# Kernel optimization log

Measured on AMD Instinct MI355X. Metric: run time of the kernel, lower is better.

The kernel has to match this reference:

```python
import jax, jax.numpy as jnp
import numpy as np

EPS = 1e-5


def setup_inputs() -> dict:
    key = jax.random.key(0)
    ks = jax.random.split(key, 7)
    B, T, H = 4, 4096, 1024
    x = jax.random.normal(ks[0], (B, T, H), dtype=jnp.float32)
    gamma = jnp.ones((H,), dtype=jnp.float32)
    beta = jnp.zeros((H,), dtype=jnp.float32)
    s = 1.0 / np.sqrt(H)
    Wg = jax.random.uniform(ks[1], (H, H), minval=-s, maxval=s, dtype=jnp.float32)
    bg = jax.random.uniform(ks[2], (H,), minval=-s, maxval=s, dtype=jnp.float32)
    Wc = jax.random.uniform(ks[3], (H, H), minval=-s, maxval=s, dtype=jnp.float32)
    bc = jax.random.uniform(ks[4], (H,), minval=-s, maxval=s, dtype=jnp.float32)
    return {"x": x, "gamma": gamma, "beta": beta, "Wg": Wg, "bg": bg, "Wc": Wc, "bc": bc}


def reference(x, gamma, beta, Wg, bg, Wc, bc):
    # x: [B, T, H]
    mu = jnp.mean(x, axis=-1, keepdims=True)
    var = jnp.mean((x - mu) ** 2, axis=-1, keepdims=True)
    normed = (x - mu) * jax.lax.rsqrt(var + EPS) * gamma + beta
    z = jax.nn.sigmoid(jnp.einsum('bth,oh->bto', normed, Wg) + bg)  # gate
    c = jnp.einsum('bth,oh->bto', normed, Wc) + bc                  # candidate
    B, T, H = x.shape

    def step(h, zc):
        z_t, c_t = zc  # each [B, H]
        h = (1.0 - z_t) * h + z_t * c_t
        return h, h

    h0 = jnp.zeros((B, H), dtype=x.dtype)
    # scan over time: move T to leading axis
    _, hs = jax.lax.scan(step, h0, (jnp.swapaxes(z, 0, 1), jnp.swapaxes(c, 0, 1)))
    return jnp.swapaxes(hs, 0, 1) + x  # residual
```

## Files before the change

### kernel.cpp

```cpp
#include <hip/hip_runtime.h>
#include <stdint.h>


#define B_    4
#define T_    4096
#define H_    1024
#define BT_   (B_*T_)
#define EPSV  1e-5f
#define CHK   128
#define CL    (T_/CHK)

typedef float  f32x4  __attribute__((ext_vector_type(4)));
typedef __bf16 bf16x8 __attribute__((ext_vector_type(8)));
typedef unsigned short u16;

__device__ __forceinline__ u16 f2bf(float f) {
  uint32_t u = __builtin_bit_cast(uint32_t, f);
  u += 0x7fffu + ((u >> 16) & 1u);
  return (u16)(u >> 16);
}
__device__ __forceinline__ float bf2f(uint32_t u) {
  uint32_t v = (u & 0xffffu) << 16;
  return __builtin_bit_cast(float, v);
}
__device__ __forceinline__ void bf4(uint2 p, float* f) {
  f[0] = bf2f(p.x); f[1] = bf2f(p.x >> 16);
  f[2] = bf2f(p.y); f[3] = bf2f(p.y >> 16);
}

__global__ __launch_bounds__(256) void ln_kernel(
    const float* __restrict__ x, const float* __restrict__ gamma,
    const float* __restrict__ beta, u16* __restrict__ normed) {
  const int wid  = threadIdx.x >> 6, lane = threadIdx.x & 63;
  const int row  = blockIdx.x * 4 + wid;
  const float4* xr = reinterpret_cast<const float4*>(x + (size_t)row * H_);
  float4 v[4];
  float s = 0.0f, q = 0.0f;
  #pragma unroll
  for (int seg = 0; seg < 4; ++seg) {
    v[seg] = xr[seg * 64 + lane];
    s += v[seg].x + v[seg].y + v[seg].z + v[seg].w;
    q += v[seg].x*v[seg].x + v[seg].y*v[seg].y + v[seg].z*v[seg].z + v[seg].w*v[seg].w;
  }
  #pragma unroll
  for (int off = 1; off < 64; off <<= 1) {
    s += __shfl_xor(s, off);
    q += __shfl_xor(q, off);
  }
  const float mean = s * (1.0f / H_);
  const float var  = q * (1.0f / H_) - mean * mean;
  const float rstd = rsqrtf(var + EPSV);
  const float4* g4 = reinterpret_cast<const float4*>(gamma);
  const float4* b4 = reinterpret_cast<const float4*>(beta);
  uint2* o2 = reinterpret_cast<uint2*>(normed + (size_t)row * H_);
  #pragma unroll
  for (int seg = 0; seg < 4; ++seg) {
    const float4 g = g4[seg * 64 + lane];
    const float4 b = b4[seg * 64 + lane];
    uint2 o;
    o.x = (uint32_t)f2bf((v[seg].x - mean) * rstd * g.x + b.x)
        | ((uint32_t)f2bf((v[seg].y - mean) * rstd * g.y + b.y) << 16);
    o.y = (uint32_t)f2bf((v[seg].z - mean) * rstd * g.z + b.z)
        | ((uint32_t)f2bf((v[seg].w - mean) * rstd * g.w + b.w) << 16);
    o2[seg * 64 + lane] = o;
  }
}

__global__ __launch_bounds__(256) void pack_kernel(
    const float* __restrict__ Wg, const float* __restrict__ Wc,
    u16* __restrict__ wpack) {
  const int idx4 = (blockIdx.x * 256 + threadIdx.x) * 4;
  const int n = idx4 >> 10;
  const int k = idx4 & 1023;
  const float* src = (n < 1024) ? (Wg + (size_t)n * 1024 + k)
                                : (Wc + (size_t)(n - 1024) * 1024 + k);
  const float4 v = *reinterpret_cast<const float4*>(src);
  uint2 o;
  o.x = (uint32_t)f2bf(v.x) | ((uint32_t)f2bf(v.y) << 16);
  o.y = (uint32_t)f2bf(v.z) | ((uint32_t)f2bf(v.w) << 16);
  *reinterpret_cast<uint2*>(wpack + idx4) = o;
}

__global__ __launch_bounds__(256) void gemm_kernel(
    const u16* __restrict__ A, const u16* __restrict__ Bw,
    const float* __restrict__ bg, const float* __restrict__ bc,
    u16* __restrict__ zbuf, u16* __restrict__ cbuf) {
  __shared__ u16 As[2][128 * 32];
  __shared__ u16 Bs[2][128 * 32];
  const int bid = blockIdx.x;
  const int nb  = (bid & 7) * 256 + (bid >> 3);
  const int mt  = nb >> 4, nt = nb & 15;
  const int tid = threadIdx.x;
  const int wid = tid >> 6, lane = tid & 63;
  const int wr = wid >> 1, wcq = wid & 1;

  f32x4 acc[4][4] = {};

  const int c0 = tid, c1 = tid + 256;
  const u16* a0 = A  + (size_t)(mt * 128 + (c0 >> 2)) * 1024 + (c0 & 3) * 8;
  const u16* a1 = A  + (size_t)(mt * 128 + (c1 >> 2)) * 1024 + (c1 & 3) * 8;
  const u16* b0 = Bw + (size_t)(nt * 128 + (c0 >> 2)) * 1024 + (c0 & 3) * 8;
  const u16* b1 = Bw + (size_t)(nt * 128 + (c1 >> 2)) * 1024 + (c1 & 3) * 8;

  const int frow = lane & 15;
  const int kb   = (lane >> 4) * 8;

  auto stage = [&](int buf, int ks) {
    const int kk = ks * 32;
    __builtin_amdgcn_global_load_lds(
        (const __attribute__((address_space(1))) void*)(a0 + kk),
        (__attribute__((address_space(3))) void*)&As[buf][c0 * 8], 16, 0, 0);
    __builtin_amdgcn_global_load_lds(
        (const __attribute__((address_space(1))) void*)(a1 + kk),
        (__attribute__((address_space(3))) void*)&As[buf][c1 * 8], 16, 0, 0);
    __builtin_amdgcn_global_load_lds(
        (const __attribute__((address_space(1))) void*)(b0 + kk),
        (__attribute__((address_space(3))) void*)&Bs[buf][c0 * 8], 16, 0, 0);
    __builtin_amdgcn_global_load_lds(
        (const __attribute__((address_space(1))) void*)(b1 + kk),
        (__attribute__((address_space(3))) void*)&Bs[buf][c1 * 8], 16, 0, 0);
  };
  auto compute = [&](int buf) {
    bf16x8 af[4], bfr[4];
    #pragma unroll
    for (int m = 0; m < 4; ++m)
      af[m] = *reinterpret_cast<const bf16x8*>(&As[buf][(wr * 64 + m * 16 + frow) * 32 + kb]);
    #pragma unroll
    for (int n = 0; n < 4; ++n)
      bfr[n] = *reinterpret_cast<const bf16x8*>(&Bs[buf][(wcq * 64 + n * 16 + frow) * 32 + kb]);
    #pragma unroll
    for (int m = 0; m < 4; ++m)
      #pragma unroll
      for (int n = 0; n < 4; ++n)
        acc[m][n] = __builtin_amdgcn_mfma_f32_16x16x32_bf16(af[m], bfr[n], acc[m][n], 0, 0, 0);
  };

  stage(0, 0);
  __syncthreads();
  int cur = 0;
  for (int ks = 0; ks < 31; ++ks) {
    stage(cur ^ 1, ks + 1);
    compute(cur);
    __syncthreads();
    cur ^= 1;
  }
  compute(cur);

  const int r0  = (lane >> 4) * 4;
  const int col16 = lane & 15;
  const bool isz = (nt < 8);
  #pragma unroll
  for (int m = 0; m < 4; ++m) {
    #pragma unroll
    for (int n = 0; n < 4; ++n) {
      const int col = nt * 128 + wcq * 64 + n * 16 + col16;
      #pragma unroll
      for (int r = 0; r < 4; ++r) {
        const int row = mt * 128 + wr * 64 + m * 16 + r0 + r;
        float v = acc[m][n][r];
        if (isz) {
          v += bg[col];
          v = 1.0f / (1.0f + __expf(-v));
          zbuf[(size_t)row * 1024 + col] = f2bf(v);
        } else {
          const int cc = col - 1024;
          v += bc[cc];
          cbuf[(size_t)row * 1024 + cc] = f2bf(v);
        }
      }
    }
  }
}

__global__ __launch_bounds__(256) void scan1_kernel(
    const u16* __restrict__ zbuf, const u16* __restrict__ cbuf,
    float* __restrict__ Achk, float* __restrict__ Uchk) {
  const int bid   = blockIdx.x;
  const int chunk = bid & (CHK - 1);
  const int b     = bid >> 7;
  const int o4    = threadIdx.x * 4;
  const size_t base = ((size_t)(b * T_ + chunk * CL)) * H_ + o4;
  float A[4] = {1.f, 1.f, 1.f, 1.f};
  float u[4] = {0.f, 0.f, 0.f, 0.f};
  #pragma unroll 4
  for (int t = 0; t < CL; ++t) {
    const size_t idx = base + (size_t)t * H_;
    const uint2 zp = *reinterpret_cast<const uint2*>(&zbuf[idx]);
    const uint2 cp = *reinterpret_cast<const uint2*>(&cbuf[idx]);
    float z[4], c[4];
    bf4(zp, z); bf4(cp, c);
    #pragma unroll
    for (int j = 0; j < 4; ++j) {
      const float a = 1.0f - z[j];
      A[j] *= a;
      u[j] = a * u[j] + z[j] * c[j];
    }
  }
  const int idx = (b * CHK + chunk) * H_ + o4;
  *reinterpret_cast<float4*>(&Achk[idx]) = make_float4(A[0], A[1], A[2], A[3]);
  *reinterpret_cast<float4*>(&Uchk[idx]) = make_float4(u[0], u[1], u[2], u[3]);
}

__global__ __launch_bounds__(256) void scan2_kernel(
    const float* __restrict__ Achk, const float* __restrict__ Uchk,
    float* __restrict__ Hin) {
  const int g = blockIdx.x * 256 + threadIdx.x;
  const int b = g >> 10;
  const int o = g & 1023;
  float h = 0.0f;
  #pragma unroll 8
  for (int j = 0; j < CHK; ++j) {
    const int idx = (b * CHK + j) * H_ + o;
    Hin[idx] = h;
    h = Achk[idx] * h + Uchk[idx];
  }
}

__global__ __launch_bounds__(256) void scan3_kernel(
    const u16* __restrict__ zbuf, const u16* __restrict__ cbuf,
    const float* __restrict__ Hin, const float* __restrict__ x,
    float* __restrict__ out) {
  const int bid   = blockIdx.x;
  const int chunk = bid & (CHK - 1);
  const int b     = bid >> 7;
  const int o4    = threadIdx.x * 4;
  const float4 hv = *reinterpret_cast<const float4*>(&Hin[(b * CHK + chunk) * H_ + o4]);
  float h[4] = {hv.x, hv.y, hv.z, hv.w};
  const size_t base = ((size_t)(b * T_ + chunk * CL)) * H_ + o4;
  #pragma unroll 4
  for (int t = 0; t < CL; ++t) {
    const size_t idx = base + (size_t)t * H_;
    const uint2 zp = *reinterpret_cast<const uint2*>(&zbuf[idx]);
    const uint2 cp = *reinterpret_cast<const uint2*>(&cbuf[idx]);
    const float4 xv = *reinterpret_cast<const float4*>(&x[idx]);
    float z[4], c[4];
    bf4(zp, z); bf4(cp, c);
    #pragma unroll
    for (int j = 0; j < 4; ++j)
      h[j] = (1.0f - z[j]) * h[j] + z[j] * c[j];
    *reinterpret_cast<float4*>(&out[idx]) =
        make_float4(h[0] + xv.x, h[1] + xv.y, h[2] + xv.z, h[3] + xv.w);
  }
}

extern "C" void kernel_launch(void* const* d_in, const int* in_sizes, int n_in,
                              void* d_out, int out_size, void* d_ws, size_t ws_size,
                              hipStream_t stream) {
  const float* x     = (const float*)d_in[0];
  const float* gamma = (const float*)d_in[1];
  const float* beta  = (const float*)d_in[2];
  const float* Wg    = (const float*)d_in[3];
  const float* bg    = (const float*)d_in[4];
  const float* Wc    = (const float*)d_in[5];
  const float* bc    = (const float*)d_in[6];
  float* out = (float*)d_out;

  char* ws = (char*)d_ws;
  u16*   normed = (u16*)(ws);
  u16*   wpack  = (u16*)(ws + 33554432ull);
  u16*   zbuf   = (u16*)(ws + 37748736ull);
  u16*   cbuf   = (u16*)(ws + 71303168ull);
  float* Achk   = (float*)(ws);
  float* Uchk   = (float*)(ws + 2097152ull);
  float* Hin    = (float*)(ws + 4194304ull);

  ln_kernel  <<<BT_/4, 256, 0, stream>>>(x, gamma, beta, normed);
  pack_kernel<<<2048,  256, 0, stream>>>(Wg, Wc, wpack);
  gemm_kernel<<<2048,  256, 0, stream>>>(normed, wpack, bg, bc, zbuf, cbuf);
  scan1_kernel<<<B_*CHK, 256, 0, stream>>>(zbuf, cbuf, Achk, Uchk);
  scan2_kernel<<<16,     256, 0, stream>>>(Achk, Uchk, Hin);
  scan3_kernel<<<B_*CHK, 256, 0, stream>>>(zbuf, cbuf, Hin, x, out);
}
```

Measured before the change: 298.3 us.

## Enlarge GEMM tile to 256x128 with swizzled LDS and double scan chunk count

The GEMM block tile grows from 128x128 to 256x128, so each warp computes 8x4 MFMA tiles and reuses its B fragments across more rows, halving the grid. LDS slots are XOR-swizzled to avoid bank conflicts on fragment reads, and launch bounds request two blocks per CU. The scan now uses 256 chunks instead of 128 for more parallelism in the scan passes, with fully unrolled inner loops. The larger accumulator array raises register pressure, which may limit occupancy or cause spills.

```diff
diff --git a/kernel.cpp b/kernel.cpp
--- a/kernel.cpp
+++ b/kernel.cpp
@@ -7,8 +7,11 @@
 #define H_    1024
 #define BT_   (B_*T_)
 #define EPSV  1e-5f
-#define CHK   128
+#define CHK   256
 #define CL    (T_/CHK)
+#define BM    256
+#define BN    128
+#define BK    32
 
 typedef float  f32x4  __attribute__((ext_vector_type(4)));
 typedef __bf16 bf16x8 __attribute__((ext_vector_type(8)));
@@ -81,58 +84,67 @@
   *reinterpret_cast<uint2*>(wpack + idx4) = o;
 }
 
-__global__ __launch_bounds__(256) void gemm_kernel(
+__global__ __launch_bounds__(256, 2) void gemm_kernel(
     const u16* __restrict__ A, const u16* __restrict__ Bw,
     const float* __restrict__ bg, const float* __restrict__ bc,
     u16* __restrict__ zbuf, u16* __restrict__ cbuf) {
-  __shared__ u16 As[2][128 * 32];
-  __shared__ u16 Bs[2][128 * 32];
+  __shared__ u16 As[2][BM * BK];
+  __shared__ u16 Bs[2][BN * BK];
   const int bid = blockIdx.x;
-  const int nb  = (bid & 7) * 256 + (bid >> 3);
+  const int nb  = (bid & 7) * 128 + (bid >> 3);
   const int mt  = nb >> 4, nt = nb & 15;
   const int tid = threadIdx.x;
   const int wid = tid >> 6, lane = tid & 63;
-  const int wr = wid >> 1, wcq = wid & 1;
-
-  f32x4 acc[4][4] = {};
-
-  const int c0 = tid, c1 = tid + 256;
-  const u16* a0 = A  + (size_t)(mt * 128 + (c0 >> 2)) * 1024 + (c0 & 3) * 8;
-  const u16* a1 = A  + (size_t)(mt * 128 + (c1 >> 2)) * 1024 + (c1 & 3) * 8;
-  const u16* b0 = Bw + (size_t)(nt * 128 + (c0 >> 2)) * 1024 + (c0 & 3) * 8;
-  const u16* b1 = Bw + (size_t)(nt * 128 + (c1 >> 2)) * 1024 + (c1 & 3) * 8;
-
+  const int wr  = wid >> 1, wcq = wid & 1;
   const int frow = lane & 15;
-  const int kb   = (lane >> 4) * 8;
+  const int physslot = (lane >> 4) ^ ((frow >> 1) & 3);
+
+  f32x4 acc[8][4] = {};
+
+  const u16* aptr[4];
+  const u16* bptr[2];
+  #pragma unroll
+  for (int i = 0; i < 4; ++i) {
+    const int c = tid + 256 * i;
+    const int row = c >> 2;
+    const int sl = (c & 3) ^ ((row >> 1) & 3);
+    aptr[i] = A + (size_t)(mt * BM + row) * 1024 + sl * 8;
+  }
+  #pragma unroll
+  for (int i = 0; i < 2; ++i) {
+    const int c = tid + 256 * i;
+    const int row = c >> 2;
+    const int sl = (c & 3) ^ ((row >> 1) & 3);
+    bptr[i] = Bw + (size_t)(nt * BN + row) * 1024 + sl * 8;
+  }
 
   auto stage = [&](int buf, int ks) {
-    const int kk = ks * 32;
-    __builtin_amdgcn_global_load_lds(
-        (const __attribute__((address_space(1))) void*)(a0 + kk),
-        (__attribute__((address_space(3))) void*)&As[buf][c0 * 8], 16, 0, 0);
-    __builtin_amdgcn_global_load_lds(
-        (const __attribute__((address_space(1))) void*)(a1 + kk),
-        (__attribute__((address_space(3))) void*)&As[buf][c1 * 8], 16, 0, 0);
-    __builtin_amdgcn_global_load_lds(
-        (const __attribute__((address_space(1))) void*)(b0 + kk),
-        (__attribute__((address_space(3))) void*)&Bs[buf][c0 * 8], 16, 0, 0);
-    __builtin_amdgcn_global_load_lds(
-        (const __attribute__((address_space(1))) void*)(b1 + kk),
-        (__attribute__((address_space(3))) void*)&Bs[buf][c1 * 8], 16, 0, 0);
+    const int kk = ks * BK;
+    #pragma unroll
+    for (int i = 0; i < 4; ++i)
+      __builtin_amdgcn_global_load_lds(
+          (const __attribute__((address_space(1))) void*)(aptr[i] + kk),
+          (__attribute__((address_space(3))) void*)&As[buf][(tid + 256 * i) * 8], 16, 0, 0);
+    #pragma unroll
+    for (int i = 0; i < 2; ++i)
+      __builtin_amdgcn_global_load_lds(
+          (const __attribute__((address_space(1))) void*)(bptr[i] + kk),
+          (__attribute__((address_space(3))) void*)&Bs[buf][(tid + 256 * i) * 8], 16, 0, 0);
   };
   auto compute = [&](int buf) {
-    bf16x8 af[4], bfr[4];
-    #pragma unroll
-    for (int m = 0; m < 4; ++m)
-      af[m] = *reinterpret_cast<const bf16x8*>(&As[buf][(wr * 64 + m * 16 + frow) * 32 + kb]);
+    bf16x8 bfr[4];
     #pragma unroll
     for (int n = 0; n < 4; ++n)
-      bfr[n] = *reinterpret_cast<const bf16x8*>(&Bs[buf][(wcq * 64 + n * 16 + frow) * 32 + kb]);
-    #pragma unroll
-    for (int m = 0; m < 4; ++m)
+      bfr[n] = *reinterpret_cast<const bf16x8*>(
+          &Bs[buf][(wcq * 64 + n * 16 + frow) * BK + physslot * 8]);
+    #pragma unroll
+    for (int m = 0; m < 8; ++m) {
+      const bf16x8 am = *reinterpret_cast<const bf16x8*>(
+          &As[buf][(wr * 128 + m * 16 + frow) * BK + physslot * 8]);
       #pragma unroll
       for (int n = 0; n < 4; ++n)
-        acc[m][n] = __builtin_amdgcn_mfma_f32_16x16x32_bf16(af[m], bfr[n], acc[m][n], 0, 0, 0);
+        acc[m][n] = __builtin_amdgcn_mfma_f32_16x16x32_bf16(am, bfr[n], acc[m][n], 0, 0, 0);
+    }
   };
 
   stage(0, 0);
@@ -146,17 +158,17 @@
   }
   compute(cur);
 
-  const int r0  = (lane >> 4) * 4;
+  const int r0 = (lane >> 4) * 4;
   const int col16 = lane & 15;
   const bool isz = (nt < 8);
   #pragma unroll
-  for (int m = 0; m < 4; ++m) {
+  for (int m = 0; m < 8; ++m) {
     #pragma unroll
     for (int n = 0; n < 4; ++n) {
-      const int col = nt * 128 + wcq * 64 + n * 16 + col16;
+      const int col = nt * BN + wcq * 64 + n * 16 + col16;
       #pragma unroll
       for (int r = 0; r < 4; ++r) {
-        const int row = mt * 128 + wr * 64 + m * 16 + r0 + r;
+        const int row = mt * BM + wr * 128 + m * 16 + r0 + r;
         float v = acc[m][n][r];
         if (isz) {
           v += bg[col];
@@ -177,12 +189,12 @@
     float* __restrict__ Achk, float* __restrict__ Uchk) {
   const int bid   = blockIdx.x;
   const int chunk = bid & (CHK - 1);
-  const int b     = bid >> 7;
+  const int b     = bid >> 8;
   const int o4    = threadIdx.x * 4;
   const size_t base = ((size_t)(b * T_ + chunk * CL)) * H_ + o4;
   float A[4] = {1.f, 1.f, 1.f, 1.f};
   float u[4] = {0.f, 0.f, 0.f, 0.f};
-  #pragma unroll 4
+  #pragma unroll
   for (int t = 0; t < CL; ++t) {
     const size_t idx = base + (size_t)t * H_;
     const uint2 zp = *reinterpret_cast<const uint2*>(&zbuf[idx]);
@@ -222,12 +234,12 @@
     float* __restrict__ out) {
   const int bid   = blockIdx.x;
   const int chunk = bid & (CHK - 1);
-  const int b     = bid >> 7;
+  const int b     = bid >> 8;
   const int o4    = threadIdx.x * 4;
   const float4 hv = *reinterpret_cast<const float4*>(&Hin[(b * CHK + chunk) * H_ + o4]);
   float h[4] = {hv.x, hv.y, hv.z, hv.w};
   const size_t base = ((size_t)(b * T_ + chunk * CL)) * H_ + o4;
-  #pragma unroll 4
+  #pragma unroll
   for (int t = 0; t < CL; ++t) {
     const size_t idx = base + (size_t)t * H_;
     const uint2 zp = *reinterpret_cast<const uint2*>(&zbuf[idx]);
@@ -261,12 +273,12 @@
   u16*   zbuf   = (u16*)(ws + 37748736ull);
   u16*   cbuf   = (u16*)(ws + 71303168ull);
   float* Achk   = (float*)(ws);
-  float* Uchk   = (float*)(ws + 2097152ull);
-  float* Hin    = (float*)(ws + 4194304ull);
+  float* Uchk   = (float*)(ws + 4194304ull);
+  float* Hin    = (float*)(ws + 8388608ull);
 
   ln_kernel  <<<BT_/4, 256, 0, stream>>>(x, gamma, beta, normed);
   pack_kernel<<<2048,  256, 0, stream>>>(Wg, Wc, wpack);
-  gemm_kernel<<<2048,  256, 0, stream>>>(normed, wpack, bg, bc, zbuf, cbuf);
+  gemm_kernel<<<1024,  256, 0, stream>>>(normed, wpack, bg, bc, zbuf, cbuf);
   scan1_kernel<<<B_*CHK, 256, 0, stream>>>(zbuf, cbuf, Achk, Uchk);
   scan2_kernel<<<16,     256, 0, stream>>>(Achk, Uchk, Hin);
   scan3_kernel<<<B_*CHK, 256, 0, stream>>>(zbuf, cbuf, Hin, x, out);
```

Measured after the change: 319.8 us. 7.2% more time.
